# Optimization experiments

Hardware: AMD Instinct MI355X
Metric: run time of the kernel (lower is better)

The kernel has to match this reference:

```python
import jax, jax.numpy as jnp
import numpy as np

N, F1, F2, D = 114, 32, 10, 100
F = F1 + F2
B = 16
EPS = 1e-5


def setup_inputs() -> dict:
    key = jax.random.key(0)
    ks = jax.random.split(key, 20)
    inp = {
        'XE_subs': jax.random.normal(ks[0], (B, 2, N, N, F), jnp.float32),
        'X_subs': jax.random.normal(ks[1], (B, 2, N, F1), jnp.float32),
        'A_subs': (jax.random.uniform(ks[2], (B, 2, N, N)) < 0.15).astype(jnp.float32),
        'XE_pros': jax.random.normal(ks[3], (B, 2, N, N, F), jnp.float32),
        'X_pros': jax.random.normal(ks[4], (B, 2, N, F1), jnp.float32),
        'A_pros': (jax.random.uniform(ks[5], (B, 2, N, N)) < 0.15).astype(jnp.float32),
        'Wi_sub': jax.random.normal(ks[6], (F, D)) * 0.1,
        'Wm1_sub': jax.random.normal(ks[7], (D, D)) * 0.1,
        'Wm2_sub': jax.random.normal(ks[8], (D, D)) * 0.1,
        'Wa_sub': jax.random.normal(ks[9], (D + F1, D)) * 0.1,
        'bn1s_g': jnp.ones((D,)), 'bn1s_b': jnp.zeros((D,)),
        'bn2s_g': jnp.ones((D,)), 'bn2s_b': jnp.zeros((D,)),
        'Wi_pro': jax.random.normal(ks[10], (F, D)) * 0.1,
        'Wm1_pro': jax.random.normal(ks[11], (D, D)) * 0.1,
        'Wm2_pro': jax.random.normal(ks[12], (D, D)) * 0.1,
        'Wa_pro': jax.random.normal(ks[13], (D + F1, D)) * 0.1,
        'bn1p_g': jnp.ones((D,)), 'bn1p_b': jnp.zeros((D,)),
        'bn2p_g': jnp.ones((D,)), 'bn2p_b': jnp.zeros((D,)),
        'bn3_g': jnp.ones((2 * D,)), 'bn3_b': jnp.zeros((2 * D,)),
        'W1': jax.random.normal(ks[14], (2 * D, 32)) * 0.07,
        'b1': jnp.zeros((32,)),
        'W2': jax.random.normal(ks[15], (32, 1)) * 0.17,
        'b2': jnp.zeros((1,)),
        'no_subs': 2, 'no_pros': 2,
    }
    return inp


def _bn4(x, g, b):
    # BatchNorm2d (training stats) over channel = last axis of [B,N,N,D]
    m = jnp.mean(x, axis=(0, 1, 2))
    v = jnp.var(x, axis=(0, 1, 2))
    return (x - m) * (g * jax.lax.rsqrt(v + EPS)) + b


def _branch(XE, X, A, no, Wi, Wm1, Wm2, Wa, g1, b1, g2, b2):
    h_max = None
    for i in range(no):
        xe = XE[:, i]                      # [B,N,N,F]
        a = A[:, i][..., None]             # [B,N,N,1]
        x = X[:, i][:, :, None, :]         # [B,N,1,F1]
        H0 = jax.nn.relu(jnp.einsum('bijf,fd->bijd', xe, Wi))  # [B,N,N,D]

        def mp(H):
            # Ones[N,N] @ transpose(H*A,1,2): column sum of (H*A) over axis 1,
            # broadcast, minus H^T, re-masked by A.
            S = jnp.sum(H * a, axis=1)                          # [B,N,D]
            return (S[:, :, None, :] - jnp.swapaxes(H, 1, 2)) * a

        H1 = jax.nn.relu(_bn4(H0 + jnp.einsum('bijd,de->bije', mp(H0), Wm1), g1, b1))
        H2 = jax.nn.relu(_bn4(H0 + jnp.einsum('bijd,de->bije', mp(H1), Wm2), g2, b2))
        Mv = jnp.sum(H2 * a, axis=2, keepdims=True)             # [B,N,1,D]
        XM = jnp.concatenate([x, Mv], axis=3)                   # [B,N,1,F1+D]
        H = jax.nn.relu(jnp.einsum('bnkf,fd->bnkd', XM, Wa))    # [B,N,1,D]
        h = jnp.sum(H[:, :, 0, :], axis=1)                      # [B,D]  (Ones1_N sum)
        h_max = h if h_max is None else jnp.maximum(h_max, h)
    return h_max


def reference(XE_subs, X_subs, A_subs, XE_pros, X_pros, A_pros,
              Wi_sub, Wm1_sub, Wm2_sub, Wa_sub, bn1s_g, bn1s_b, bn2s_g, bn2s_b,
              Wi_pro, Wm1_pro, Wm2_pro, Wa_pro, bn1p_g, bn1p_b, bn2p_g, bn2p_b,
              bn3_g, bn3_b, W1, b1, W2, b2, no_subs, no_pros):
    h_sub = _branch(XE_subs, X_subs, A_subs, int(no_subs),
                    Wi_sub, Wm1_sub, Wm2_sub, Wa_sub, bn1s_g, bn1s_b, bn2s_g, bn2s_b)
    h_pro = _branch(XE_pros, X_pros, A_pros, int(no_pros),
                    Wi_pro, Wm1_pro, Wm2_pro, Wa_pro, bn1p_g, bn1p_b, bn2p_g, bn2p_b)
    h = jnp.concatenate([h_sub, h_pro], axis=1)                 # [B,2D]
    m = jnp.mean(h, axis=0)
    v = jnp.var(h, axis=0)
    h = (h - m) * (bn3_g * jax.lax.rsqrt(v + EPS)) + bn3_b      # BatchNorm1d
    h = jax.nn.relu(h @ W1 + b1)
    return h @ W2 + b2                                          # [B,1]
```

## Files before the change

kernel.cpp:

```cpp
#include <hip/hip_runtime.h>

#define NN_ 114
#define NSQ (114*114)
#define FF 42
#define F1_ 32
#define DD 100
#define BB 16
#define ROWS (BB*NSQ)
#define NT512 407
#define MAXE 2432
#define NEB (MAXE/64)
#define MAXR 3968
#define EPS 1e-5f

typedef __attribute__((ext_vector_type(8))) short short8;
typedef __attribute__((ext_vector_type(4))) float f32x4;

static __device__ inline short f2bf(float f) {
    unsigned u;
    __builtin_memcpy(&u, &f, 4);
    unsigned r = (u + 0x7FFFu + ((u >> 16) & 1u)) >> 16;
    return (short)r;
}

__global__ __launch_bounds__(1024) void k_edges(const float* __restrict__ Aa0,
                                                const float* __restrict__ Aa1,
                                                int* __restrict__ Eij, int* __restrict__ Idx,
                                                int* __restrict__ Ridx, int* __restrict__ Rlist,
                                                int* __restrict__ cnt, int* __restrict__ rcnt) {
    int b = blockIdx.x, combo = blockIdx.y;
    int zb = combo*BB + b;
    const float* am = ((combo < 2) ? Aa0 : Aa1) + (long)(b*2 + (combo & 1))*NSQ;
    int tid = threadIdx.x;
    __shared__ unsigned long long m0[NN_], m1[NN_];
    __shared__ int base_e, base_u;
    __shared__ int we[16], wu[16];
    int lane = tid & 63, wv = tid >> 6;
    if (tid == 0) { base_e = 0; base_u = 0; }
    for (int i = wv; i < NN_; i += 16) {
        float v0 = am[i*NN_ + lane];
        unsigned long long w0 = __ballot(v0 != 0.f);
        float v1 = (lane < NN_-64) ? am[i*NN_ + 64 + lane] : 0.f;
        unsigned long long w1 = __ballot(v1 != 0.f);
        if (lane == 0) { m0[i] = w0; m1[i] = w1; }
    }
    __syncthreads();
    for (int c0 = 0; c0 < NSQ; c0 += 1024) {
        int idx = c0 + tid;
        bool pe = false, pu = false;
        if (idx < NSQ) {
            int ii = idx / NN_, jj = idx - ii*NN_;
            pe = (((jj < 64 ? (m0[ii] >> jj) : (m1[ii] >> (jj-64))) & 1ull) != 0);
            bool pt = (((ii < 64 ? (m0[jj] >> ii) : (m1[jj] >> (ii-64))) & 1ull) != 0);
            pu = pe || pt;
        }
        unsigned long long me = __ballot(pe), mu = __ballot(pu);
        if (lane == 0) { we[wv] = __popcll(me); wu[wv] = __popcll(mu); }
        __syncthreads();
        int oe = base_e, ou = base_u;
        for (int w = 0; w < wv; w++) { oe += we[w]; ou += wu[w]; }
        oe += __popcll(me & ((1ull << lane) - 1ull));
        ou += __popcll(mu & ((1ull << lane) - 1ull));
        if (idx < NSQ) {
            bool oke = pe && (oe < MAXE);
            Idx[(long)zb*NSQ + idx]  = oke ? oe : -1;
            if (oke) Eij[zb*MAXE + oe] = idx;
            bool oku = pu && (ou < MAXR);
            Ridx[(long)zb*NSQ + idx] = oku ? ou : -1;
            if (oku) Rlist[(long)zb*MAXR + ou] = idx;
        }
        __syncthreads();
        if (tid == 0) { for (int w = 0; w < 16; w++) { base_e += we[w]; base_u += wu[w]; } }
        __syncthreads();
    }
    if (tid == 0) {
        cnt[zb]  = (base_e < MAXE) ? base_e : MAXE;
        rcnt[zb] = (base_u < MAXR) ? base_u : MAXR;
    }
}

__global__ __launch_bounds__(256) void k_h0stat(const float* __restrict__ XE0,
                                                const float* __restrict__ XE1,
                                                const float* __restrict__ Wi0,
                                                const float* __restrict__ Wi1,
                                                float* __restrict__ P0) {
    __shared__ char smem[16384 + 14336];
    char* Abase = smem;
    char* Bbase = smem + 16384;
    int tid = threadIdx.x;
    int combo = blockIdx.y;
    const float* XE = (combo < 2) ? XE0 : XE1;
    const float* Wi = (combo < 2) ? Wi0 : Wi1;
    int slot = combo & 1;
    for (int c = tid; c < 896; c += 256) {
        int col = c >> 3, k8b = (c & 7) * 8;
        short8 pk;
#pragma unroll
        for (int t = 0; t < 8; t++) {
            int k = k8b + t;
            pk[t] = (col < DD && k < FF) ? f2bf(Wi[k*DD + col]) : (short)0;
        }
        int byte = (col*128 + k8b*2) ^ ((col & 7) << 4);
        *reinterpret_cast<short8*>(Bbase + byte) = pk;
    }
    int w = tid >> 6, l = tid & 63;
    int lr = l & 15, g = l >> 4;
    float psum[7], psq[7];
#pragma unroll
    for (int ct = 0; ct < 7; ct++) { psum[ct] = 0.f; psq[ct] = 0.f; }
    int k8 = (tid & 7) * 8;
    int rbase = tid >> 3;
    for (int sub = 0; sub < 4; sub++) {
        int tileRow = blockIdx.x * 512 + sub * 128;
        float av[4][8];
#pragma unroll
        for (int c4 = 0; c4 < 4; c4++) {
            int r = tileRow + rbase + c4*32;
            if (r < ROWS && k8 < FF) {
                int b = r / NSQ;
                int ij = r - b*NSQ;
                const float* src = XE + ((long)(b*2 + slot)*NSQ + ij)*FF + k8;
                if (k8 <= 32) {
#pragma unroll
                    for (int q = 0; q < 4; q++) {
                        float2 f = *reinterpret_cast<const float2*>(src + q*2);
                        av[c4][q*2] = f.x; av[c4][q*2+1] = f.y;
                    }
                } else {
                    float2 f = *reinterpret_cast<const float2*>(src);
                    av[c4][0] = f.x; av[c4][1] = f.y;
#pragma unroll
                    for (int q = 2; q < 8; q++) av[c4][q] = 0.f;
                }
            } else {
#pragma unroll
                for (int q = 0; q < 8; q++) av[c4][q] = 0.f;
            }
        }
        __syncthreads();
#pragma unroll
        for (int c4 = 0; c4 < 4; c4++) {
            int row = rbase + c4*32;
            short8 pk;
#pragma unroll
            for (int t = 0; t < 8; t++) pk[t] = f2bf(av[c4][t]);
            int byte = (row*128 + k8*2) ^ ((row & 7) << 4);
            *reinterpret_cast<short8*>(Abase + byte) = pk;
        }
        __syncthreads();
        short8 af[2][2];
#pragma unroll
        for (int rt = 0; rt < 2; rt++) {
            int row = (w*2 + rt)*16 + lr;
#pragma unroll
            for (int kf = 0; kf < 2; kf++) {
                int byte = (row*128 + kf*64 + g*16) ^ ((row & 7) << 4);
                af[rt][kf] = *reinterpret_cast<const short8*>(Abase + byte);
            }
        }
#pragma unroll
        for (int ct = 0; ct < 7; ct++) {
            int col = ct*16 + lr;
            int bb0 = (col*128 +  0 + g*16) ^ ((col & 7) << 4);
            int bb1 = (col*128 + 64 + g*16) ^ ((col & 7) << 4);
            short8 bf0 = *reinterpret_cast<const short8*>(Bbase + bb0);
            short8 bf1 = *reinterpret_cast<const short8*>(Bbase + bb1);
            f32x4 a0 = (f32x4){0.f,0.f,0.f,0.f};
            f32x4 a1 = (f32x4){0.f,0.f,0.f,0.f};
            a0 = __builtin_amdgcn_mfma_f32_16x16x32_bf16(af[0][0], bf0, a0, 0, 0, 0);
            a0 = __builtin_amdgcn_mfma_f32_16x16x32_bf16(af[0][1], bf1, a0, 0, 0, 0);
            a1 = __builtin_amdgcn_mfma_f32_16x16x32_bf16(af[1][0], bf0, a1, 0, 0, 0);
            a1 = __builtin_amdgcn_mfma_f32_16x16x32_bf16(af[1][1], bf1, a1, 0, 0, 0);
#pragma unroll
            for (int rr = 0; rr < 4; rr++) {
                float v0 = fmaxf(a0[rr], 0.f);
                float v1 = fmaxf(a1[rr], 0.f);
                psum[ct] += v0 + v1;
                psq[ct]  += v0*v0 + v1*v1;
            }
        }
    }
    __syncthreads();
    float* red_s = (float*)smem;
    float* red_q = red_s + 16*112;
    int idx16 = w*4 + g;
#pragma unroll
    for (int ct = 0; ct < 7; ct++) {
        red_s[idx16*112 + ct*16 + lr] = psum[ct];
        red_q[idx16*112 + ct*16 + lr] = psq[ct];
    }
    __syncthreads();
    if (tid < DD) {
        float s = 0.f, q = 0.f;
#pragma unroll
        for (int t2 = 0; t2 < 16; t2++) { s += red_s[t2*112 + tid]; q += red_q[t2*112 + tid]; }
        P0[((long)combo*NT512 + blockIdx.x)*200 + tid] = s;
        P0[((long)combo*NT512 + blockIdx.x)*200 + 100 + tid] = q;
    }
}

__global__ __launch_bounds__(256) void k_h0u(const float* __restrict__ XE0,
                                             const float* __restrict__ XE1,
                                             const float* __restrict__ Wi0,
                                             const float* __restrict__ Wi1,
                                             const int* __restrict__ Rlist,
                                             const int* __restrict__ rcnt,
                                             float* __restrict__ H0c, int zbase) {
    __shared__ float smem[FF*68 + FF*112];
    float* As = smem;
    float* Bs = smem + FF*68;
    __shared__ int srcOff[64];
    int tid = threadIdx.x;
    int b = blockIdx.y, z = blockIdx.z;
    int combo = zbase + z;
    const float* XE = (combo < 2) ? XE0 : XE1;
    const float* Wi = (combo < 2) ? Wi0 : Wi1;
    int slot = combo & 1;
    int zbE = combo*BB + b;
    int zbH = z*BB + b;
    int rid0 = blockIdx.x * 64;
    int rc = rcnt[zbE];
    if (rid0 >= rc) return;
    if (tid < 64) {
        int rid = rid0 + tid;
        int ij = (rid < rc) ? Rlist[(long)zbE*MAXR + rid] : Rlist[(long)zbE*MAXR];
        srcOff[tid] = ((b*2+slot)*NSQ + ij)*FF;
    }
    for (int idx = tid; idx < FF*112; idx += 256) {
        int kk = idx / 112, col = idx - kk*112;
        Bs[idx] = (col < DD) ? Wi[kk*DD + col] : 0.f;
    }
    __syncthreads();
    for (int idx = tid; idx < 64*FF; idx += 256) {
        int rr = idx / FF, kk = idx - rr*FF;
        As[kk*68 + rr] = XE[(long)srcOff[rr] + kk];
    }
    int ty = tid >> 4, tx = tid & 15;
    float acc[4][7];
#pragma unroll
    for (int i = 0; i < 4; i++)
#pragma unroll
        for (int j = 0; j < 7; j++) acc[i][j] = 0.f;
    __syncthreads();
    for (int kk = 0; kk < FF; kk++) {
        float4 avv = *reinterpret_cast<const float4*>(&As[kk*68 + ty*4]);
#pragma unroll
        for (int cc = 0; cc < 7; cc++) {
            float bv = Bs[kk*112 + tx + 16*cc];
            acc[0][cc] += avv.x*bv; acc[1][cc] += avv.y*bv;
            acc[2][cc] += avv.z*bv; acc[3][cc] += avv.w*bv;
        }
    }
#pragma unroll
    for (int rq = 0; rq < 4; rq++) {
        int rid = rid0 + ty*4 + rq;
        if (rid < rc) {
#pragma unroll
            for (int cc = 0; cc < 7; cc++) {
                int col = tx + 16*cc;
                if (col < DD)
                    H0c[((long)zbH*MAXR + rid)*DD + col] = fmaxf(acc[rq][cc], 0.f);
            }
        }
    }
}

template<int LAYER>
__global__ __launch_bounds__(128) void k_cs(const float* __restrict__ H0c,
                                            const int* __restrict__ Idx,
                                            const int* __restrict__ Ridx,
                                            const float* __restrict__ Dprev,
                                            const float* __restrict__ bnsc,
                                            float* __restrict__ CSp, int zbase) {
    int bi = blockIdx.x, part = blockIdx.y, z = blockIdx.z;
    int b = bi / NN_, i = bi % NN_;
    int zbE = (zbase + z)*BB + b;
    int zbH = z*BB + b;
    int k0 = part*29, k1 = (k0+29 < NN_) ? k0+29 : NN_;
    __shared__ int eid_s[29], row_s[29];
    int tid = threadIdx.x;
    if (tid < k1-k0) {
        long pos = (long)zbE*NSQ + (k0+tid)*NN_ + i;
        eid_s[tid] = Idx[pos];
        row_s[tid] = Ridx[pos];
    }
    __syncthreads();
    if (tid < DD) {
        float sc = 0.f, sh = 0.f;
        if (LAYER == 2) { sc = bnsc[z*200 + tid]; sh = bnsc[z*200 + DD + tid]; }
        float acc = 0.f;
        for (int k = 0; k < k1-k0; k++) {
            int e = eid_s[k];
            if (e >= 0) {
                float v = H0c[((long)zbH*MAXR + row_s[k])*DD + tid];
                if (LAYER == 2) { v += Dprev[((long)zbH*MAXE + e)*DD + tid]; v = fmaxf(v*sc+sh, 0.f); }
                acc += v;
            }
        }
        CSp[(((long)z*BB*NN_ + bi)*4 + part)*DD + tid] = acc;
    }
}

__global__ __launch_bounds__(256) void k_swgemm(const float* __restrict__ CSp,
                                                const float* __restrict__ W0,
                                                const float* __restrict__ W1,
                                                float* __restrict__ SW, int zbase) {
    const int M = BB*NN_;
    __shared__ float smem[50*68 + 50*DD];
    float* As = smem;
    float* Bs = smem + 50*68;
    int tid = threadIdx.x;
    int z = blockIdx.y;
    const float* W = ((zbase + z) < 2) ? W0 : W1;
    const float* In = CSp + (long)z*M*4*DD;
    float* Out = SW + (long)z*M*DD;
    int tileRow = blockIdx.x * 64;
    int ty = tid >> 4, tx = tid & 15;
    float acc[4][7];
#pragma unroll
    for (int i=0;i<4;i++)
#pragma unroll
        for (int j=0;j<7;j++) acc[i][j]=0.f;
    for (int kc = 0; kc < 2; kc++) {
        __syncthreads();
        for (int idx = tid; idx < 64*50; idx += 256) {
            int rr = idx / 50, kk = idx % 50;
            int r = tileRow + rr;
            float v = 0.f;
            if (r < M) {
                long base = (long)r*4*DD + kc*50 + kk;
                v = In[base] + In[base+DD] + In[base+2*DD] + In[base+3*DD];
            }
            As[kk*68 + rr] = v;
        }
        for (int idx = tid; idx < 50*DD; idx += 256) {
            int kk = idx / DD, e = idx % DD;
            Bs[kk*DD + e] = W[(kc*50+kk)*DD + e];
        }
        __syncthreads();
        for (int kk = 0; kk < 50; kk++) {
            float4 av = *reinterpret_cast<const float4*>(&As[kk*68 + ty*4]);
#pragma unroll
            for (int cc=0; cc<7; cc++) {
                int col = tx + 16*cc;
                float bv = (col < DD) ? Bs[kk*DD + col] : 0.f;
                acc[0][cc] += av.x*bv; acc[1][cc] += av.y*bv;
                acc[2][cc] += av.z*bv; acc[3][cc] += av.w*bv;
            }
        }
    }
#pragma unroll
    for (int rq=0;rq<4;rq++){
        int r = tileRow + ty*4 + rq;
        if (r < M) {
#pragma unroll
            for (int cc=0;cc<7;cc++){
                int col = tx+16*cc;
                if (col < DD) Out[(long)r*DD + col] = acc[rq][cc];
            }
        }
    }
}

template<int LAYER>
__global__ __launch_bounds__(256) void k_dcomb(const float* __restrict__ H0c,
                                               const int* __restrict__ Eij,
                                               const int* __restrict__ cnt,
                                               const int* __restrict__ Idx,
                                               const int* __restrict__ Ridx,
                                               const float* __restrict__ Dprev,
                                               const float* __restrict__ Wm0,
                                               const float* __restrict__ Wm1,
                                               const float* __restrict__ SW,
                                               const float* __restrict__ bnsc,
                                               float* __restrict__ Dout,
                                               float* __restrict__ PD, int zbase) {
    __shared__ float smem[50*68 + 50*DD];
    float* As = smem;
    float* Bs = smem + 50*68;
    __shared__ int srcOff[64], addOff[64], h0Off[64], swOff[64];
    __shared__ float s1[DD], t1[DD];
    int tid = threadIdx.x;
    int b = blockIdx.y, z = blockIdx.z;
    int combo = zbase + z;
    const float* Wm = (combo < 2) ? Wm0 : Wm1;
    int zbE = combo*BB + b;
    int zbH = z*BB + b;
    int e0 = blockIdx.x * 64;
    int c = cnt[zbE];
    long pdbase = ((long)zbH*NEB + blockIdx.x)*200;
    if (e0 >= c) {
        if (tid < DD) { PD[pdbase + tid] = 0.f; PD[pdbase + 100 + tid] = 0.f; }
        return;
    }
    if (LAYER == 2 && tid < DD) { s1[tid]=bnsc[z*200+tid]; t1[tid]=bnsc[z*200+DD+tid]; }
    if (tid < 64) {
        int e = e0 + tid;
        if (e < c) {
            int ij = Eij[zbE*MAXE + e];
            int ii = ij / NN_, jj = ij % NN_;
            long tpos = (long)zbE*NSQ + jj*NN_ + ii;
            srcOff[tid] = (zbH*MAXR + Ridx[tpos])*DD;
            h0Off[tid]  = (zbH*MAXR + Ridx[(long)zbE*NSQ + ij])*DD;
            swOff[tid]  = ((z*BB + b)*NN_ + ii)*DD;
            if (LAYER == 2) {
                int et = Idx[tpos];
                addOff[tid] = (et >= 0) ? (zbH*MAXE + et)*DD : -1;
            } else addOff[tid] = -1;
        } else { srcOff[tid]=0; h0Off[tid]=0; swOff[tid]=0; addOff[tid]=-1; }
    }
    int ty = tid >> 4, tx = tid & 15;
    float acc[4][7];
#pragma unroll
    for (int i=0;i<4;i++)
#pragma unroll
        for (int j=0;j<7;j++) acc[i][j]=0.f;
    for (int kc = 0; kc < 2; kc++) {
        __syncthreads();
        for (int idx = tid; idx < 64*50; idx += 256) {
            int rr = idx / 50, kk = idx % 50;
            float v = H0c[(long)srcOff[rr] + kc*50 + kk];
            if (LAYER == 2) {
                if (addOff[rr] >= 0) v += Dprev[(long)addOff[rr] + kc*50 + kk];
                v = fmaxf(v*s1[kc*50+kk] + t1[kc*50+kk], 0.f);
            }
            As[kk*68 + rr] = v;
        }
        for (int idx = tid; idx < 50*DD; idx += 256) {
            int kk = idx / DD, e = idx % DD;
            Bs[kk*DD + e] = Wm[(kc*50+kk)*DD + e];
        }
        __syncthreads();
        for (int kk = 0; kk < 50; kk++) {
            float4 av = *reinterpret_cast<const float4*>(&As[kk*68 + ty*4]);
#pragma unroll
            for (int cc=0; cc<7; cc++) {
                int col = tx + 16*cc;
                float bv = (col < DD) ? Bs[kk*DD + col] : 0.f;
                acc[0][cc] += av.x*bv; acc[1][cc] += av.y*bv;
                acc[2][cc] += av.z*bv; acc[3][cc] += av.w*bv;
            }
        }
    }
    float psum[7], psq[7];
#pragma unroll
    for (int cc=0;cc<7;cc++){psum[cc]=0.f;psq[cc]=0.f;}
#pragma unroll
    for (int rq=0; rq<4; rq++) {
        int rr = ty*4 + rq;
        int e = e0 + rr;
        if (e < c) {
            long doff = ((long)zbH*MAXE + e)*DD;
#pragma unroll
            for (int cc=0;cc<7;cc++) {
                int col = tx+16*cc;
                if (col < DD) {
                    float d = SW[swOff[rr] + col] - acc[rq][cc];
                    Dout[doff + col] = d;
                    float h = H0c[(long)h0Off[rr] + col];
                    psum[cc] += d;
                    psq[cc]  += (2.f*h + d)*d;
                }
            }
        }
    }
    __syncthreads();
    float* red_s = smem;
    float* red_q = smem + 16*112;
#pragma unroll
    for (int cc=0;cc<7;cc++) {
        int col = tx+16*cc;
        red_s[ty*112+col] = psum[cc];
        red_q[ty*112+col] = psq[cc];
    }
    __syncthreads();
    if (tid < DD) {
        float s=0.f,q=0.f;
#pragma unroll
        for (int t2=0;t2<16;t2++){ s+=red_s[t2*112+tid]; q+=red_q[t2*112+tid]; }
        PD[pdbase + tid] = s;
        PD[pdbase + 100 + tid] = q;
    }
}

__global__ __launch_bounds__(256) void k_bnfin(const float* __restrict__ P0,
                                               const float* __restrict__ PD,
                                               const float* __restrict__ g0,
                                               const float* __restrict__ g1,
                                               const float* __restrict__ bb0,
                                               const float* __restrict__ bb1,
                                               float* __restrict__ bnsc, int zbase) {
    __shared__ float rs[256], rq[256];
    int e = blockIdx.x, z = blockIdx.y;
    int combo = zbase + z;
    const float* g  = (combo < 2) ? g0  : g1;
    const float* bb = (combo < 2) ? bb0 : bb1;
    int tid = threadIdx.x;
    const float* P = PD + (long)z*BB*NEB*200;
    float s=0.f,q=0.f;
    for (int p=tid; p<BB*NEB; p+=256){ s += P[(long)p*200 + e]; q += P[(long)p*200 + 100 + e]; }
    const float* PP = P0 + (long)combo*NT512*200;
    for (int p=tid; p<NT512; p+=256){ s += PP[(long)p*200 + e]; q += PP[(long)p*200 + 100 + e]; }
    rs[tid]=s; rq[tid]=q; __syncthreads();
    for (int off=128; off>0; off>>=1){
        if (tid<off){ rs[tid]+=rs[tid+off]; rq[tid]+=rq[tid+off]; }
        __syncthreads();
    }
    if (tid==0){
        float m = rs[0]/(float)ROWS;
        float var = rq[0]/(float)ROWS - m*m;
        float sc = g[e]*rsqrtf(var+EPS);
        bnsc[z*200 + e] = sc;
        bnsc[z*200 + DD + e] = bb[e] - m*sc;
    }
}

__global__ __launch_bounds__(128) void k_mvxm(const float* __restrict__ H0c,
                                              const int* __restrict__ Idx,
                                              const int* __restrict__ Ridx,
                                              const float* __restrict__ D2,
                                              const float* __restrict__ bnsc,
                                              const float* __restrict__ X0,
                                              const float* __restrict__ X1,
                                              const float* __restrict__ Wa0,
                                              const float* __restrict__ Wa1,
                                              float* __restrict__ hpart, int zbase) {
    int n = blockIdx.x, b = blockIdx.y, z = blockIdx.z;
    int combo = zbase + z;
    const float* X  = (combo < 2) ? X0  : X1;
    const float* Wa = (combo < 2) ? Wa0 : Wa1;
    int slot = combo & 1;
    int zbE = combo*BB + b;
    int zbH = z*BB + b;
    int tid = threadIdx.x;
    __shared__ int eid_s[NN_], row_s[NN_];
    __shared__ float xm[132];
    if (tid < NN_) {
        long pos = (long)zbE*NSQ + n*NN_ + tid;
        eid_s[tid] = Idx[pos];
        row_s[tid] = Ridx[pos];
    }
    if (tid < F1_) xm[tid] = X[((long)(b*2+slot)*NN_ + n)*F1_ + tid];
    __syncthreads();
    if (tid < DD) {
        float sc = bnsc[z*200+tid], sh = bnsc[z*200+DD+tid];
        float acc = 0.f;
        for (int j = 0; j < NN_; j++) {
            int e = eid_s[j];
            if (e >= 0) {
                float v = H0c[((long)zbH*MAXR + row_s[j])*DD + tid]
                        + D2[((long)zbH*MAXE + e)*DD + tid];
                acc += fmaxf(v*sc + sh, 0.f);
            }
        }
        xm[F1_ + tid] = acc;
    }
    __syncthreads();
    if (tid < DD) {
        float acc = 0.f;
        for (int f = 0; f < 132; f++) acc += xm[f]*Wa[f*DD + tid];
        hpart[(((long)combo*BB + b)*NN_ + n)*DD + tid] = fmaxf(acc, 0.f);
    }
}

__global__ __launch_bounds__(128) void k_hred(const float* __restrict__ hpart,
                                              float* __restrict__ h) {
    int cb = blockIdx.x;
    int tid = threadIdx.x;
    if (tid < DD) {
        float acc = 0.f;
        for (int n = 0; n < NN_; n++) acc += hpart[((long)cb*NN_ + n)*DD + tid];
        h[(long)cb*DD + tid] = acc;
    }
}

__global__ __launch_bounds__(256) void k_head(const float* __restrict__ h,
                                              const float* __restrict__ g3, const float* __restrict__ b3,
                                              const float* __restrict__ W1, const float* __restrict__ b1,
                                              const float* __restrict__ W2, const float* __restrict__ b2,
                                              float* __restrict__ out) {
    __shared__ float hl[BB][200];
    __shared__ float z[BB][32];
    int tid = threadIdx.x;
    for (int idx=tid; idx<BB*200; idx+=256){
        int b = idx/200, c = idx%200;
        float v;
        if (c < DD) v = fmaxf(h[(0*BB+b)*DD + c],        h[(1*BB+b)*DD + c]);
        else        v = fmaxf(h[(2*BB+b)*DD + (c-DD)],   h[(3*BB+b)*DD + (c-DD)]);
        hl[b][c] = v;
    }
    __syncthreads();
    if (tid < 200){
        float m=0.f;
        for (int b=0;b<BB;b++) m += hl[b][tid];
        m *= (1.f/BB);
        float v=0.f;
        for (int b=0;b<BB;b++){ float d = hl[b][tid]-m; v += d*d; }
        v *= (1.f/BB);
        float sc = g3[tid]*rsqrtf(v+EPS);
        float sh = b3[tid] - m*sc;
        for (int b=0;b<BB;b++) hl[b][tid] = hl[b][tid]*sc + sh;
    }
    __syncthreads();
    for (int idx=tid; idx<BB*32; idx+=256){
        int b = idx/32, k = idx%32;
        float accv = b1[k];
        for (int c=0;c<200;c++) accv += hl[b][c]*W1[c*32+k];
        z[b][k] = fmaxf(accv, 0.f);
    }
    __syncthreads();
    if (tid < BB){
        float accv = b2[0];
        for (int k=0;k<32;k++) accv += z[tid][k]*W2[k];
        out[tid] = accv;
    }
}

extern "C" void kernel_launch(void* const* d_in, const int* in_sizes, int n_in,
                              void* d_out, int out_size, void* d_ws, size_t ws_size,
                              hipStream_t stream) {
    const float* XE[2]  = {(const float*)d_in[0],  (const float*)d_in[3]};
    const float* Xi[2]  = {(const float*)d_in[1],  (const float*)d_in[4]};
    const float* Aa[2]  = {(const float*)d_in[2],  (const float*)d_in[5]};
    const float* Wi[2]  = {(const float*)d_in[6],  (const float*)d_in[14]};
    const float* Wm1[2] = {(const float*)d_in[7],  (const float*)d_in[15]};
    const float* Wm2[2] = {(const float*)d_in[8],  (const float*)d_in[16]};
    const float* Wa[2]  = {(const float*)d_in[9],  (const float*)d_in[17]};
    const float* g1[2]  = {(const float*)d_in[10], (const float*)d_in[18]};
    const float* bb1[2] = {(const float*)d_in[11], (const float*)d_in[19]};
    const float* g2[2]  = {(const float*)d_in[12], (const float*)d_in[20]};
    const float* bb2[2] = {(const float*)d_in[13], (const float*)d_in[21]};

    const long perNC  = (long)BB*MAXR*DD + 2L*BB*MAXE*DD + (long)BB*NN_*4*DD
                      + (long)BB*NN_*DD + (long)BB*NEB*200;
    const long fixedF = 4L*NT512*200 + 2048 + 4L*BB*NN_*DD + 6400;
    const long intsN  = 4L*BB*MAXE + 8L*BB*NSQ + 4L*BB*MAXR + 128;
    int NC = (ws_size >= (size_t)(4L*perNC + fixedF + intsN) * 4) ? 4 : 2;

    float* p = (float*)d_ws;
    float* H0c = p;  p += (long)NC*BB*MAXR*DD;
    float* D1  = p;  p += (long)NC*BB*MAXE*DD;
    float* D2  = p;  p += (long)NC*BB*MAXE*DD;
    float* CSp = p;  p += (long)NC*BB*NN_*4*DD;
    float* SW  = p;  p += (long)NC*BB*NN_*DD;
    float* PD  = p;  p += (long)NC*BB*NEB*200;
    float* P0  = p;  p += 4L*NT512*200;
    float* bns1= p;  p += 1024;
    float* bns2= p;  p += 1024;
    float* hpart=p;  p += 4L*BB*NN_*DD;
    float* h   = p;  p += 6400;
    int* Eij   = (int*)p;
    int* Idx   = Eij  + 4*BB*MAXE;
    int* Ridx  = Idx  + 4*BB*NSQ;
    int* Rlist = Ridx + 4*BB*NSQ;
    int* cnt   = Rlist + 4*BB*MAXR;
    int* rcnt  = cnt + 64;

    k_edges<<<dim3(BB, 4), 1024, 0, stream>>>(Aa[0], Aa[1], Eij, Idx, Ridx, Rlist, cnt, rcnt);
    k_h0stat<<<dim3(NT512, 4), 256, 0, stream>>>(XE[0], XE[1], Wi[0], Wi[1], P0);

    for (int g = 0; g < 4; g += NC) {
        k_h0u<<<dim3(MAXR/64, BB, NC), 256, 0, stream>>>(XE[0], XE[1], Wi[0], Wi[1],
                                                         Rlist, rcnt, H0c, g);
        k_cs<1><<<dim3(BB*NN_, 4, NC), 128, 0, stream>>>(H0c, Idx, Ridx, nullptr, nullptr, CSp, g);
        k_swgemm<<<dim3(29, NC), 256, 0, stream>>>(CSp, Wm1[0], Wm1[1], SW, g);
        k_dcomb<1><<<dim3(NEB, BB, NC), 256, 0, stream>>>(H0c, Eij, cnt, Idx, Ridx, nullptr,
                                                          Wm1[0], Wm1[1], SW, nullptr, D1, PD, g);
        k_bnfin<<<dim3(DD, NC), 256, 0, stream>>>(P0, PD, g1[0], g1[1], bb1[0], bb1[1], bns1, g);
        k_cs<2><<<dim3(BB*NN_, 4, NC), 128, 0, stream>>>(H0c, Idx, Ridx, D1, bns1, CSp, g);
        k_swgemm<<<dim3(29, NC), 256, 0, stream>>>(CSp, Wm2[0], Wm2[1], SW, g);
        k_dcomb<2><<<dim3(NEB, BB, NC), 256, 0, stream>>>(H0c, Eij, cnt, Idx, Ridx, D1,
                                                          Wm2[0], Wm2[1], SW, bns1, D2, PD, g);
        k_bnfin<<<dim3(DD, NC), 256, 0, stream>>>(P0, PD, g2[0], g2[1], bb2[0], bb2[1], bns2, g);
        k_mvxm<<<dim3(NN_, BB, NC), 128, 0, stream>>>(H0c, Idx, Ridx, D2, bns2,
                                                      Xi[0], Xi[1], Wa[0], Wa[1], hpart, g);
    }
    k_hred<<<4*BB, 128, 0, stream>>>(hpart, h);
    k_head<<<1, 256, 0, stream>>>(h,
        (const float*)d_in[22], (const float*)d_in[23],
        (const float*)d_in[24], (const float*)d_in[25],
        (const float*)d_in[26], (const float*)d_in[27],
        (float*)d_out);
}
```

Baseline: 494.7 us.

## Use split-bf16 MFMA for the message-passing GEMM in k_dcomb

Replaces the scalar FP32 64x100x100 GEMM in k_dcomb with bf16 MFMA 16x16x32 instructions. Each operand is split into hi and lo bf16 parts and accumulated with three MFMAs to keep near-FP32 accuracy. Operands are staged in XOR-swizzled LDS, and the epilogue is remapped to the MFMA output layout. This trades FP32 ALU work for matrix-core throughput, at the cost of extra conversion work and a small precision risk.

```diff
diff --git a/kernel.cpp b/kernel.cpp
--- a/kernel.cpp
+++ b/kernel.cpp
@@ -21,6 +21,12 @@
     __builtin_memcpy(&u, &f, 4);
     unsigned r = (u + 0x7FFFu + ((u >> 16) & 1u)) >> 16;
     return (short)r;
+}
+static __device__ inline float bf2f(short h) {
+    unsigned u = ((unsigned)(unsigned short)h) << 16;
+    float f;
+    __builtin_memcpy(&f, &u, 4);
+    return f;
 }
 
 __global__ __launch_bounds__(1024) void k_edges(const float* __restrict__ Aa0,
@@ -375,9 +381,11 @@
                                                const float* __restrict__ bnsc,
                                                float* __restrict__ Dout,
                                                float* __restrict__ PD, int zbase) {
-    __shared__ float smem[50*68 + 50*DD];
-    float* As = smem;
-    float* Bs = smem + 50*68;
+    __shared__ char smem[45056];
+    char* Ahi = smem;
+    char* Alo = smem + 8192;
+    char* Bhi = smem + 16384;
+    char* Blo = smem + 16384 + 14336;
     __shared__ int srcOff[64], addOff[64], h0Off[64], swOff[64];
     __shared__ float s1[DD], t1[DD];
     int tid = threadIdx.x;
@@ -409,75 +417,113 @@
             } else addOff[tid] = -1;
         } else { srcOff[tid]=0; h0Off[tid]=0; swOff[tid]=0; addOff[tid]=-1; }
     }
-    int ty = tid >> 4, tx = tid & 15;
-    float acc[4][7];
-#pragma unroll
-    for (int i=0;i<4;i++)
-#pragma unroll
-        for (int j=0;j<7;j++) acc[i][j]=0.f;
+    int w = tid >> 6, l = tid & 63;
+    int lr = l & 15, g = l >> 4;
+    f32x4 acc[7];
+#pragma unroll
+    for (int ct = 0; ct < 7; ct++) acc[ct] = (f32x4){0.f,0.f,0.f,0.f};
     for (int kc = 0; kc < 2; kc++) {
         __syncthreads();
-        for (int idx = tid; idx < 64*50; idx += 256) {
-            int rr = idx / 50, kk = idx % 50;
-            float v = H0c[(long)srcOff[rr] + kc*50 + kk];
-            if (LAYER == 2) {
-                if (addOff[rr] >= 0) v += Dprev[(long)addOff[rr] + kc*50 + kk];
-                v = fmaxf(v*s1[kc*50+kk] + t1[kc*50+kk], 0.f);
-            }
-            As[kk*68 + rr] = v;
-        }
-        for (int idx = tid; idx < 50*DD; idx += 256) {
-            int kk = idx / DD, e = idx % DD;
-            Bs[kk*DD + e] = Wm[(kc*50+kk)*DD + e];
-        }
-        __syncthreads();
-        for (int kk = 0; kk < 50; kk++) {
-            float4 av = *reinterpret_cast<const float4*>(&As[kk*68 + ty*4]);
-#pragma unroll
-            for (int cc=0; cc<7; cc++) {
-                int col = tx + 16*cc;
-                float bv = (col < DD) ? Bs[kk*DD + col] : 0.f;
-                acc[0][cc] += av.x*bv; acc[1][cc] += av.y*bv;
-                acc[2][cc] += av.z*bv; acc[3][cc] += av.w*bv;
+        for (int idx = tid; idx < 512; idx += 256) {
+            int row = idx >> 3, k8 = (idx & 7) * 8;
+            int kbase = kc*64 + k8;
+            const float* src = H0c + srcOff[row] + kbase;
+            const float* dsrc = (LAYER == 2 && addOff[row] >= 0) ? (Dprev + addOff[row] + kbase) : nullptr;
+            short8 hi, lo;
+#pragma unroll
+            for (int t = 0; t < 8; t++) {
+                int k = kbase + t;
+                float x = 0.f;
+                if (k < DD) {
+                    x = src[t];
+                    if (LAYER == 2) {
+                        if (dsrc) x += dsrc[t];
+                        x = fmaxf(x*s1[k] + t1[k], 0.f);
+                    }
+                }
+                short h = f2bf(x);
+                hi[t] = h;
+                lo[t] = f2bf(x - bf2f(h));
+            }
+            int byte = (row*128 + k8*2) ^ ((row & 7) << 4);
+            *reinterpret_cast<short8*>(Ahi + byte) = hi;
+            *reinterpret_cast<short8*>(Alo + byte) = lo;
+        }
+        for (int idx = tid; idx < 896; idx += 256) {
+            int col = idx >> 3, k8 = (idx & 7) * 8;
+            short8 hi, lo;
+#pragma unroll
+            for (int t = 0; t < 8; t++) {
+                int k = kc*64 + k8 + t;
+                float x = (col < DD && k < DD) ? Wm[k*DD + col] : 0.f;
+                short h = f2bf(x);
+                hi[t] = h;
+                lo[t] = f2bf(x - bf2f(h));
+            }
+            int byte = (col*128 + k8*2) ^ ((col & 7) << 4);
+            *reinterpret_cast<short8*>(Bhi + byte) = hi;
+            *reinterpret_cast<short8*>(Blo + byte) = lo;
+        }
+        __syncthreads();
+        int arow = w*16 + lr;
+        short8 ah[2], al[2];
+#pragma unroll
+        for (int kf = 0; kf < 2; kf++) {
+            int byte = (arow*128 + kf*64 + g*16) ^ ((arow & 7) << 4);
+            ah[kf] = *reinterpret_cast<const short8*>(Ahi + byte);
+            al[kf] = *reinterpret_cast<const short8*>(Alo + byte);
+        }
+#pragma unroll
+        for (int ct = 0; ct < 7; ct++) {
+            int col = ct*16 + lr;
+#pragma unroll
+            for (int kf = 0; kf < 2; kf++) {
+                int byte = (col*128 + kf*64 + g*16) ^ ((col & 7) << 4);
+                short8 bh = *reinterpret_cast<const short8*>(Bhi + byte);
+                short8 bl = *reinterpret_cast<const short8*>(Blo + byte);
+                acc[ct] = __builtin_amdgcn_mfma_f32_16x16x32_bf16(ah[kf], bh, acc[ct], 0, 0, 0);
+                acc[ct] = __builtin_amdgcn_mfma_f32_16x16x32_bf16(ah[kf], bl, acc[ct], 0, 0, 0);
+                acc[ct] = __builtin_amdgcn_mfma_f32_16x16x32_bf16(al[kf], bh, acc[ct], 0, 0, 0);
             }
         }
     }
     float psum[7], psq[7];
 #pragma unroll
-    for (int cc=0;cc<7;cc++){psum[cc]=0.f;psq[cc]=0.f;}
-#pragma unroll
-    for (int rq=0; rq<4; rq++) {
-        int rr = ty*4 + rq;
-        int e = e0 + rr;
+    for (int ct = 0; ct < 7; ct++) { psum[ct] = 0.f; psq[ct] = 0.f; }
+#pragma unroll
+    for (int reg = 0; reg < 4; reg++) {
+        int rloc = w*16 + g*4 + reg;
+        int e = e0 + rloc;
         if (e < c) {
             long doff = ((long)zbH*MAXE + e)*DD;
-#pragma unroll
-            for (int cc=0;cc<7;cc++) {
-                int col = tx+16*cc;
+            int swo = swOff[rloc], h0o = h0Off[rloc];
+#pragma unroll
+            for (int ct = 0; ct < 7; ct++) {
+                int col = ct*16 + lr;
                 if (col < DD) {
-                    float d = SW[swOff[rr] + col] - acc[rq][cc];
+                    float d = SW[swo + col] - acc[ct][reg];
                     Dout[doff + col] = d;
-                    float h = H0c[(long)h0Off[rr] + col];
-                    psum[cc] += d;
-                    psq[cc]  += (2.f*h + d)*d;
+                    float hh = H0c[h0o + col];
+                    psum[ct] += d;
+                    psq[ct]  += (2.f*hh + d)*d;
                 }
             }
         }
     }
     __syncthreads();
-    float* red_s = smem;
-    float* red_q = smem + 16*112;
-#pragma unroll
-    for (int cc=0;cc<7;cc++) {
-        int col = tx+16*cc;
-        red_s[ty*112+col] = psum[cc];
-        red_q[ty*112+col] = psq[cc];
+    float* red_s = (float*)smem;
+    float* red_q = red_s + 16*112;
+    int idx16 = w*4 + g;
+#pragma unroll
+    for (int ct = 0; ct < 7; ct++) {
+        red_s[idx16*112 + ct*16 + lr] = psum[ct];
+        red_q[idx16*112 + ct*16 + lr] = psq[ct];
     }
     __syncthreads();
     if (tid < DD) {
-        float s=0.f,q=0.f;
-#pragma unroll
-        for (int t2=0;t2<16;t2++){ s+=red_s[t2*112+tid]; q+=red_q[t2*112+tid]; }
+        float s = 0.f, q = 0.f;
+#pragma unroll
+        for (int t2 = 0; t2 < 16; t2++) { s += red_s[t2*112 + tid]; q += red_q[t2*112 + tid]; }
         PD[pdbase + tid] = s;
         PD[pdbase + 100 + tid] = q;
     }
```

After: 475.1 us. 1.04x faster.
